# Kernel tuning notes

Measured on AMD Instinct MI355X. Metric: run time of the kernel, lower is better.

Reference implementation:

```python
import jax, jax.numpy as jnp
import numpy as np

N = 200000          # graph_size (stalk rows)
H = 128             # hidden_channels
NNZ = 3200000       # Laplacian nnz (avg degree 16)
K = 15              # polynomial degree (poly_layers_K)
LAMBDA_MAX = 2.0    # normalised Laplacian -> analytic lambda_max


def setup_inputs() -> dict:
    key = jax.random.key(0)
    ks = jax.random.split(key, 6)
    x = jax.random.normal(ks[0], (N, H), dtype=jnp.float32)
    vals = jax.random.normal(ks[1], (NNZ,), dtype=jnp.float32)
    poly_logits = jax.random.normal(ks[2], (K + 1,), dtype=jnp.float32)
    hp_alpha = jax.random.normal(ks[3], (), dtype=jnp.float32)
    edge_row = jax.random.randint(ks[4], (NNZ,), 0, N, dtype=jnp.int64)
    edge_col = jax.random.randint(ks[5], (NNZ,), 0, N, dtype=jnp.int64)
    return {"x": x, "vals": vals, "poly_logits": poly_logits,
            "hp_alpha": hp_alpha, "edge_row": edge_row, "edge_col": edge_col}


def reference(x, vals, poly_logits, hp_alpha, edge_row, edge_col):
    n = x.shape[0]

    def spmm(v):  # (n,h) -> (n,h), sparse L @ v in COO form
        return jax.ops.segment_sum(vals[:, None] * v[edge_col], edge_row,
                                   num_segments=n)

    def Lhat(v):  # L_hat = (2/lambda_max) L - I
        return (2.0 / LAMBDA_MAX) * spmm(v) - v

    w = jax.nn.softmax(poly_logits)  # mixture over Chebyshev T_0..T_K

    # Chebyshev Type-1 recurrence: T_{k+1} = 2 L_hat T_k - T_{k-1}
    T0 = x
    T1 = Lhat(x)
    out = w[0] * T0 + w[1] * T1

    def step(carry, wk):
        T0, T1, out = carry
        Tk1 = 2.0 * Lhat(T1) - T0
        return (T1, Tk1, out + wk * Tk1), None

    (_, _, px), _ = jax.lax.scan(step, (T0, T1, out), w[2:])

    # high-pass term: x - (1/lambda_max) L x
    hp = x - spmm(x) / LAMBDA_MAX
    return -px + hp_alpha * hp
```

## Files before the change

### kernel.cpp

```cpp
#include <hip/hip_runtime.h>
#include <math.h>

#define N_NODES 200000
#define H_CH    128
#define NNZ_E   3200000
#define K_DEG   15

__global__ void softmax_k(const float* __restrict__ logits, float* __restrict__ w) {
    if (threadIdx.x == 0) {
        float m = -1e30f;
        for (int i = 0; i <= K_DEG; ++i) m = fmaxf(m, logits[i]);
        float e[K_DEG + 1];
        float s = 0.f;
        for (int i = 0; i <= K_DEG; ++i) { e[i] = expf(logits[i] - m); s += e[i]; }
        float inv = 1.0f / s;
        for (int i = 0; i <= K_DEG; ++i) w[i] = e[i] * inv;
    }
}

__global__ void hist_k(const int* __restrict__ row, int* __restrict__ counts, int nnz) {
    int i = blockIdx.x * blockDim.x + threadIdx.x;
    if (i < nnz) atomicAdd(&counts[row[i]], 1);
}

__global__ void scan1_k(const int* __restrict__ counts, int* __restrict__ out,
                        int* __restrict__ partials, int n) {
    __shared__ int sm[256];
    int tbase = blockIdx.x * 2048 + threadIdx.x * 8;
    int v[8];
    int tsum = 0;
#pragma unroll
    for (int j = 0; j < 8; ++j) {
        int i = tbase + j;
        int c = (i < n) ? counts[i] : 0;
        v[j] = tsum;
        tsum += c;
    }
    sm[threadIdx.x] = tsum;
    __syncthreads();
    int incl = tsum;
    for (int off = 1; off < 256; off <<= 1) {
        int t = (threadIdx.x >= (unsigned)off) ? sm[threadIdx.x - off] : 0;
        __syncthreads();
        incl += t;
        sm[threadIdx.x] = incl;
        __syncthreads();
    }
    int texcl = incl - tsum;
    if (threadIdx.x == 255) partials[blockIdx.x] = incl;
#pragma unroll
    for (int j = 0; j < 8; ++j) {
        int i = tbase + j;
        if (i < n) out[i] = texcl + v[j];
    }
}

__global__ void scan2_k(int* partials, int nb, int* row_ptr, int n, int total) {
    __shared__ int sm[128];
    int v = (threadIdx.x < (unsigned)nb) ? partials[threadIdx.x] : 0;
    sm[threadIdx.x] = v;
    __syncthreads();
    int incl = v;
    for (int off = 1; off < 128; off <<= 1) {
        int t = (threadIdx.x >= (unsigned)off) ? sm[threadIdx.x - off] : 0;
        __syncthreads();
        incl += t;
        sm[threadIdx.x] = incl;
        __syncthreads();
    }
    if (threadIdx.x < (unsigned)nb) partials[threadIdx.x] = incl - v;
    if (threadIdx.x == 0) row_ptr[n] = total;
}

__global__ void scan3_k(int* __restrict__ row_ptr, const int* __restrict__ partials,
                        int* __restrict__ fill, int n) {
    int off = partials[blockIdx.x];
    int tbase = blockIdx.x * 2048 + threadIdx.x * 8;
#pragma unroll
    for (int j = 0; j < 8; ++j) {
        int i = tbase + j;
        if (i < n) {
            int v = row_ptr[i] + off;
            row_ptr[i] = v;
            fill[i] = v;
        }
    }
}

__global__ void scatter_k(const int* __restrict__ row, const int* __restrict__ col,
                          const float* __restrict__ vals, int* __restrict__ fill,
                          int* __restrict__ ccol, float* __restrict__ cval, int nnz) {
    int i = blockIdx.x * blockDim.x + threadIdx.x;
    if (i < nnz) {
        int r = row[i];
        int p = atomicAdd(&fill[r], 1);
        ccol[p] = col[i];
        cval[p] = vals[i];
    }
}

__global__ __launch_bounds__(256) void first_k(
    const int* __restrict__ rp, const int* __restrict__ ccol, const float* __restrict__ cval,
    const float* __restrict__ x, float* __restrict__ T1buf, float* __restrict__ out,
    const float* __restrict__ w, const float* __restrict__ alpha_p) {
    int wid = blockIdx.x * 4 + (threadIdx.x >> 6);
    int r = __builtin_amdgcn_readfirstlane(wid);
    if (r >= N_NODES) return;
    int lane = threadIdx.x & 63;
    const float* base = x + lane * 2;
    int e0 = rp[r], e1 = rp[r + 1];
    float ax = 0.f, ay = 0.f, bx = 0.f, by = 0.f;
    int e = e0;
    for (; e + 2 <= e1; e += 2) {
        int c0 = ccol[e], c1 = ccol[e + 1];
        float v0 = cval[e], v1 = cval[e + 1];
        float2 s0 = *(const float2*)(base + (size_t)c0 * H_CH);
        float2 s1 = *(const float2*)(base + (size_t)c1 * H_CH);
        ax = fmaf(v0, s0.x, ax); ay = fmaf(v0, s0.y, ay);
        bx = fmaf(v1, s1.x, bx); by = fmaf(v1, s1.y, by);
    }
    if (e < e1) {
        int c0 = ccol[e];
        float v0 = cval[e];
        float2 s0 = *(const float2*)(base + (size_t)c0 * H_CH);
        ax = fmaf(v0, s0.x, ax); ay = fmaf(v0, s0.y, ay);
    }
    float sx = ax + bx, sy = ay + by;
    size_t idx = (size_t)r * H_CH + lane * 2;
    float2 xr = *(const float2*)(x + idx);
    float w0 = w[0], w1 = w[1], al = alpha_p[0];
    float t1x = sx - xr.x, t1y = sy - xr.y;
    float ox = -(w0 * xr.x + w1 * t1x) + al * (xr.x - 0.5f * sx);
    float oy = -(w0 * xr.y + w1 * t1y) + al * (xr.y - 0.5f * sy);
    float2 t1v; t1v.x = t1x; t1v.y = t1y;
    float2 ov;  ov.x = ox;   ov.y = oy;
    *(float2*)(T1buf + idx) = t1v;
    *(float2*)(out + idx) = ov;
}

__global__ __launch_bounds__(256) void cheb_k(
    const int* __restrict__ rp, const int* __restrict__ ccol, const float* __restrict__ cval,
    const float* __restrict__ Tcur, const float* Tprev, float* Tnext,
    float* __restrict__ out, const float* __restrict__ w, int k) {
    int wid = blockIdx.x * 4 + (threadIdx.x >> 6);
    int r = __builtin_amdgcn_readfirstlane(wid);
    if (r >= N_NODES) return;
    int lane = threadIdx.x & 63;
    const float* base = Tcur + lane * 2;
    int e0 = rp[r], e1 = rp[r + 1];
    float ax = 0.f, ay = 0.f, bx = 0.f, by = 0.f;
    int e = e0;
    for (; e + 2 <= e1; e += 2) {
        int c0 = ccol[e], c1 = ccol[e + 1];
        float v0 = cval[e], v1 = cval[e + 1];
        float2 s0 = *(const float2*)(base + (size_t)c0 * H_CH);
        float2 s1 = *(const float2*)(base + (size_t)c1 * H_CH);
        ax = fmaf(v0, s0.x, ax); ay = fmaf(v0, s0.y, ay);
        bx = fmaf(v1, s1.x, bx); by = fmaf(v1, s1.y, by);
    }
    if (e < e1) {
        int c0 = ccol[e];
        float v0 = cval[e];
        float2 s0 = *(const float2*)(base + (size_t)c0 * H_CH);
        ax = fmaf(v0, s0.x, ax); ay = fmaf(v0, s0.y, ay);
    }
    float sx = ax + bx, sy = ay + by;
    size_t idx = (size_t)r * H_CH + lane * 2;
    float2 tc = *(const float2*)(Tcur + idx);
    float2 tp = *(const float2*)(Tprev + idx);
    float wk = w[k];
    float tnx = 2.0f * (sx - tc.x) - tp.x;
    float tny = 2.0f * (sy - tc.y) - tp.y;
    float2 ov = *(const float2*)(out + idx);
    ov.x -= wk * tnx;
    ov.y -= wk * tny;
    *(float2*)(out + idx) = ov;
    float2 tn; tn.x = tnx; tn.y = tny;
    *(float2*)(Tnext + idx) = tn;
}

extern "C" void kernel_launch(void* const* d_in, const int* in_sizes, int n_in,
                              void* d_out, int out_size, void* d_ws, size_t ws_size,
                              hipStream_t stream) {
    const float* x      = (const float*)d_in[0];
    const float* vals   = (const float*)d_in[1];
    const float* logits = (const float*)d_in[2];
    const float* alpha  = (const float*)d_in[3];
    const int*   erow   = (const int*)d_in[4];
    const int*   ecol   = (const int*)d_in[5];
    float* out = (float*)d_out;

    const size_t NH = (size_t)N_NODES * H_CH;
    float* bufA    = (float*)d_ws;
    float* bufB    = bufA + NH;
    int*   csr_col = (int*)(bufB + NH);
    float* csr_val = (float*)(csr_col + NNZ_E);
    int*   row_ptr = (int*)(csr_val + NNZ_E);
    int*   counts  = row_ptr + (N_NODES + 1);
    int*   fill    = counts + N_NODES;
    int*   partials= fill + N_NODES;
    float* w_buf   = (float*)(partials + 128);

    hipMemsetAsync(counts, 0, N_NODES * sizeof(int), stream);
    softmax_k<<<1, 64, 0, stream>>>(logits, w_buf);
    hist_k<<<(NNZ_E + 255) / 256, 256, 0, stream>>>(erow, counts, NNZ_E);

    const int TILE = 2048;
    int nblk = (N_NODES + TILE - 1) / TILE;
    scan1_k<<<nblk, 256, 0, stream>>>(counts, row_ptr, partials, N_NODES);
    scan2_k<<<1, 128, 0, stream>>>(partials, nblk, row_ptr, N_NODES, NNZ_E);
    scan3_k<<<nblk, 256, 0, stream>>>(row_ptr, partials, fill, N_NODES);
    scatter_k<<<(NNZ_E + 255) / 256, 256, 0, stream>>>(erow, ecol, vals, fill,
                                                       csr_col, csr_val, NNZ_E);

    int grid = (N_NODES + 3) / 4;
    first_k<<<grid, 256, 0, stream>>>(row_ptr, csr_col, csr_val, x, bufB, out, w_buf, alpha);

    cheb_k<<<grid, 256, 0, stream>>>(row_ptr, csr_col, csr_val, bufB, x, bufA, out, w_buf, 2);

    float* Tcur = bufA;
    float* Tprev = bufB;
    for (int k = 3; k <= K_DEG; ++k) {
        cheb_k<<<grid, 256, 0, stream>>>(row_ptr, csr_col, csr_val, Tcur, Tprev, Tprev,
                                         out, w_buf, k);
        float* t = Tcur; Tcur = Tprev; Tprev = t;
    }
}
```

Measured before the change: 4.755 ms.

## Split channels into two 64-wide groups and pack CSR col/val pairs

Runs the Chebyshev recurrence separately for each half of the hidden channels, halving the T buffer footprint so the gathered working set is more cache-resident. CSR column indices and values are packed into one int2 array, and the edge loop is unrolled by four with independent accumulators. The cost is reading the CSR structure twice, doubling kernel launches, and narrower per-row gathers.

```diff
diff --git a/kernel.cpp b/kernel.cpp
--- a/kernel.cpp
+++ b/kernel.cpp
@@ -3,6 +3,7 @@
 
 #define N_NODES 200000
 #define H_CH    128
+#define GRP     64
 #define NNZ_E   3200000
 #define K_DEG   15
 
@@ -89,94 +90,87 @@
 
 __global__ void scatter_k(const int* __restrict__ row, const int* __restrict__ col,
                           const float* __restrict__ vals, int* __restrict__ fill,
-                          int* __restrict__ ccol, float* __restrict__ cval, int nnz) {
+                          int2* __restrict__ csr, int nnz) {
     int i = blockIdx.x * blockDim.x + threadIdx.x;
     if (i < nnz) {
         int r = row[i];
         int p = atomicAdd(&fill[r], 1);
-        ccol[p] = col[i];
-        cval[p] = vals[i];
+        int2 cv;
+        cv.x = col[i];
+        cv.y = __float_as_int(vals[i]);
+        csr[p] = cv;
     }
 }
 
 __global__ __launch_bounds__(256) void first_k(
-    const int* __restrict__ rp, const int* __restrict__ ccol, const float* __restrict__ cval,
-    const float* __restrict__ x, float* __restrict__ T1buf, float* __restrict__ out,
-    const float* __restrict__ w, const float* __restrict__ alpha_p) {
+    const int* __restrict__ rp, const int2* __restrict__ csr,
+    const float* __restrict__ x, float* __restrict__ T1g, float* __restrict__ out,
+    const float* __restrict__ w, const float* __restrict__ alpha_p, int goff) {
     int wid = blockIdx.x * 4 + (threadIdx.x >> 6);
     int r = __builtin_amdgcn_readfirstlane(wid);
     if (r >= N_NODES) return;
     int lane = threadIdx.x & 63;
-    const float* base = x + lane * 2;
+    const float* base = x + goff + lane;
     int e0 = rp[r], e1 = rp[r + 1];
-    float ax = 0.f, ay = 0.f, bx = 0.f, by = 0.f;
+    float a0 = 0.f, a1 = 0.f, a2 = 0.f, a3 = 0.f;
     int e = e0;
-    for (; e + 2 <= e1; e += 2) {
-        int c0 = ccol[e], c1 = ccol[e + 1];
-        float v0 = cval[e], v1 = cval[e + 1];
-        float2 s0 = *(const float2*)(base + (size_t)c0 * H_CH);
-        float2 s1 = *(const float2*)(base + (size_t)c1 * H_CH);
-        ax = fmaf(v0, s0.x, ax); ay = fmaf(v0, s0.y, ay);
-        bx = fmaf(v1, s1.x, bx); by = fmaf(v1, s1.y, by);
-    }
-    if (e < e1) {
-        int c0 = ccol[e];
-        float v0 = cval[e];
-        float2 s0 = *(const float2*)(base + (size_t)c0 * H_CH);
-        ax = fmaf(v0, s0.x, ax); ay = fmaf(v0, s0.y, ay);
-    }
-    float sx = ax + bx, sy = ay + by;
-    size_t idx = (size_t)r * H_CH + lane * 2;
-    float2 xr = *(const float2*)(x + idx);
+    for (; e + 4 <= e1; e += 4) {
+        int2 cv0 = csr[e], cv1 = csr[e + 1], cv2 = csr[e + 2], cv3 = csr[e + 3];
+        a0 = fmaf(__int_as_float(cv0.y), base[(size_t)cv0.x * H_CH], a0);
+        a1 = fmaf(__int_as_float(cv1.y), base[(size_t)cv1.x * H_CH], a1);
+        a2 = fmaf(__int_as_float(cv2.y), base[(size_t)cv2.x * H_CH], a2);
+        a3 = fmaf(__int_as_float(cv3.y), base[(size_t)cv3.x * H_CH], a3);
+    }
+    for (; e < e1; ++e) {
+        int2 cv = csr[e];
+        a0 = fmaf(__int_as_float(cv.y), base[(size_t)cv.x * H_CH], a0);
+    }
+    float s = (a0 + a1) + (a2 + a3);
+    size_t idxg = (size_t)r * GRP + lane;
+    size_t idxf = (size_t)r * H_CH + goff + lane;
+    float xr = x[idxf];
     float w0 = w[0], w1 = w[1], al = alpha_p[0];
-    float t1x = sx - xr.x, t1y = sy - xr.y;
-    float ox = -(w0 * xr.x + w1 * t1x) + al * (xr.x - 0.5f * sx);
-    float oy = -(w0 * xr.y + w1 * t1y) + al * (xr.y - 0.5f * sy);
-    float2 t1v; t1v.x = t1x; t1v.y = t1y;
-    float2 ov;  ov.x = ox;   ov.y = oy;
-    *(float2*)(T1buf + idx) = t1v;
-    *(float2*)(out + idx) = ov;
+    float t1 = s - xr;
+    float o = -(w0 * xr + w1 * t1) + al * (xr - 0.5f * s);
+    T1g[idxg] = t1;
+    out[idxf] = o;
 }
 
 __global__ __launch_bounds__(256) void cheb_k(
-    const int* __restrict__ rp, const int* __restrict__ ccol, const float* __restrict__ cval,
-    const float* __restrict__ Tcur, const float* Tprev, float* Tnext,
-    float* __restrict__ out, const float* __restrict__ w, int k) {
+    const int* __restrict__ rp, const int2* __restrict__ csr,
+    const float* __restrict__ Tcur, const float* TprevBase, int tprevStride,
+    float* Tnext, float* __restrict__ out,
+    const float* __restrict__ w, int k, int goff) {
     int wid = blockIdx.x * 4 + (threadIdx.x >> 6);
     int r = __builtin_amdgcn_readfirstlane(wid);
     if (r >= N_NODES) return;
     int lane = threadIdx.x & 63;
-    const float* base = Tcur + lane * 2;
+    const float* base = Tcur + lane;
     int e0 = rp[r], e1 = rp[r + 1];
-    float ax = 0.f, ay = 0.f, bx = 0.f, by = 0.f;
+    float a0 = 0.f, a1 = 0.f, a2 = 0.f, a3 = 0.f;
     int e = e0;
-    for (; e + 2 <= e1; e += 2) {
-        int c0 = ccol[e], c1 = ccol[e + 1];
-        float v0 = cval[e], v1 = cval[e + 1];
-        float2 s0 = *(const float2*)(base + (size_t)c0 * H_CH);
-        float2 s1 = *(const float2*)(base + (size_t)c1 * H_CH);
-        ax = fmaf(v0, s0.x, ax); ay = fmaf(v0, s0.y, ay);
-        bx = fmaf(v1, s1.x, bx); by = fmaf(v1, s1.y, by);
-    }
-    if (e < e1) {
-        int c0 = ccol[e];
-        float v0 = cval[e];
-        float2 s0 = *(const float2*)(base + (size_t)c0 * H_CH);
-        ax = fmaf(v0, s0.x, ax); ay = fmaf(v0, s0.y, ay);
-    }
-    float sx = ax + bx, sy = ay + by;
-    size_t idx = (size_t)r * H_CH + lane * 2;
-    float2 tc = *(const float2*)(Tcur + idx);
-    float2 tp = *(const float2*)(Tprev + idx);
+    for (; e + 4 <= e1; e += 4) {
+        int2 cv0 = csr[e], cv1 = csr[e + 1], cv2 = csr[e + 2], cv3 = csr[e + 3];
+        a0 = fmaf(__int_as_float(cv0.y), base[(size_t)cv0.x * GRP], a0);
+        a1 = fmaf(__int_as_float(cv1.y), base[(size_t)cv1.x * GRP], a1);
+        a2 = fmaf(__int_as_float(cv2.y), base[(size_t)cv2.x * GRP], a2);
+        a3 = fmaf(__int_as_float(cv3.y), base[(size_t)cv3.x * GRP], a3);
+    }
+    for (; e < e1; ++e) {
+        int2 cv = csr[e];
+        a0 = fmaf(__int_as_float(cv.y), base[(size_t)cv.x * GRP], a0);
+    }
+    float s = (a0 + a1) + (a2 + a3);
+    size_t idxg = (size_t)r * GRP + lane;
+    size_t idxf = (size_t)r * H_CH + goff + lane;
+    float tc = Tcur[idxg];
+    float tp = TprevBase[(size_t)r * tprevStride + lane];
     float wk = w[k];
-    float tnx = 2.0f * (sx - tc.x) - tp.x;
-    float tny = 2.0f * (sy - tc.y) - tp.y;
-    float2 ov = *(const float2*)(out + idx);
-    ov.x -= wk * tnx;
-    ov.y -= wk * tny;
-    *(float2*)(out + idx) = ov;
-    float2 tn; tn.x = tnx; tn.y = tny;
-    *(float2*)(Tnext + idx) = tn;
+    float tn = 2.0f * (s - tc) - tp;
+    float o = out[idxf];
+    o -= wk * tn;
+    out[idxf] = o;
+    Tnext[idxg] = tn;
 }
 
 extern "C" void kernel_launch(void* const* d_in, const int* in_sizes, int n_in,
@@ -190,12 +184,11 @@
     const int*   ecol   = (const int*)d_in[5];
     float* out = (float*)d_out;
 
-    const size_t NH = (size_t)N_NODES * H_CH;
+    const size_t NG = (size_t)N_NODES * GRP;
     float* bufA    = (float*)d_ws;
-    float* bufB    = bufA + NH;
-    int*   csr_col = (int*)(bufB + NH);
-    float* csr_val = (float*)(csr_col + NNZ_E);
-    int*   row_ptr = (int*)(csr_val + NNZ_E);
+    float* bufB    = bufA + NG;
+    int2*  csr     = (int2*)(bufB + NG);
+    int*   row_ptr = (int*)(csr + NNZ_E);
     int*   counts  = row_ptr + (N_NODES + 1);
     int*   fill    = counts + N_NODES;
     int*   partials= fill + N_NODES;
@@ -210,19 +203,21 @@
     scan1_k<<<nblk, 256, 0, stream>>>(counts, row_ptr, partials, N_NODES);
     scan2_k<<<1, 128, 0, stream>>>(partials, nblk, row_ptr, N_NODES, NNZ_E);
     scan3_k<<<nblk, 256, 0, stream>>>(row_ptr, partials, fill, N_NODES);
-    scatter_k<<<(NNZ_E + 255) / 256, 256, 0, stream>>>(erow, ecol, vals, fill,
-                                                       csr_col, csr_val, NNZ_E);
+    scatter_k<<<(NNZ_E + 255) / 256, 256, 0, stream>>>(erow, ecol, vals, fill, csr, NNZ_E);
 
     int grid = (N_NODES + 3) / 4;
-    first_k<<<grid, 256, 0, stream>>>(row_ptr, csr_col, csr_val, x, bufB, out, w_buf, alpha);
-
-    cheb_k<<<grid, 256, 0, stream>>>(row_ptr, csr_col, csr_val, bufB, x, bufA, out, w_buf, 2);
-
-    float* Tcur = bufA;
-    float* Tprev = bufB;
-    for (int k = 3; k <= K_DEG; ++k) {
-        cheb_k<<<grid, 256, 0, stream>>>(row_ptr, csr_col, csr_val, Tcur, Tprev, Tprev,
-                                         out, w_buf, k);
-        float* t = Tcur; Tcur = Tprev; Tprev = t;
-    }
-}
+
+    for (int g = 0; g < H_CH / GRP; ++g) {
+        int goff = g * GRP;
+        first_k<<<grid, 256, 0, stream>>>(row_ptr, csr, x, bufB, out, w_buf, alpha, goff);
+        cheb_k<<<grid, 256, 0, stream>>>(row_ptr, csr, bufB, x + goff, H_CH, bufA,
+                                         out, w_buf, 2, goff);
+        float* Tcur = bufA;
+        float* Tprev = bufB;
+        for (int k = 3; k <= K_DEG; ++k) {
+            cheb_k<<<grid, 256, 0, stream>>>(row_ptr, csr, Tcur, Tprev, GRP, Tprev,
+                                             out, w_buf, k, goff);
+            float* t = Tcur; Tcur = Tprev; Tprev = t;
+        }
+    }
+}
```

New measurement: 4.703 ms. About the same (-1.1%).
